# Performance work log

Measured on AMD Instinct MI355X. Metric: run time of the kernel, lower is better.

The kernel has to match this reference:

```python
import jax, jax.numpy as jnp
import numpy as np

N_NODES = 100000
N_EDGES = 1600000
DIM = 128


def setup_inputs() -> dict:
    key = jax.random.key(0)
    k_x, k_e, k_wm, k_bm, k_wu, k_bu = jax.random.split(key, 6)
    bound = 1.0 / np.sqrt(DIM)
    return {
        "x": jax.random.normal(k_x, (N_NODES, DIM), dtype=jnp.float32),
        "edge_index": jax.random.randint(k_e, (2, N_EDGES), 0, N_NODES, dtype=jnp.int64),
        "W_msg": jax.random.uniform(k_wm, (DIM, DIM), jnp.float32, -bound, bound),
        "b_msg": jax.random.uniform(k_bm, (DIM,), jnp.float32, -bound, bound),
        "W_upd": jax.random.uniform(k_wu, (DIM, DIM), jnp.float32, -bound, bound),
        "b_upd": jax.random.uniform(k_bu, (DIM,), jnp.float32, -bound, bound),
    }


def reference(x, edge_index, W_msg, b_msg, W_upd, b_upd):
    # message_net: Linear + ReLU on all nodes  [N, D]
    messages = jax.nn.relu(x @ W_msg.T + b_msg)
    src, dst = edge_index[0], edge_index[1]
    # gather by src, scatter-add by dst (index_add)  [N, D]
    aggregated = jax.ops.segment_sum(messages[src], dst, num_segments=x.shape[0])
    # update_net: Linear + ReLU, then residual
    updated = jax.nn.relu(aggregated @ W_upd.T + b_upd)
    return updated + x
```

## Files before the change

### kernel.cpp

```cpp
#include <hip/hip_runtime.h>
#include <hip/hip_bf16.h>

#define DIM 128
#define BNODES 64
#define CNODES 1024
#define NCMAX 128
#define NBMAX 2048
#define CCAP 20480
#define BCAP 2048
#define FB 16

typedef __attribute__((ext_vector_type(8))) short bf16x8;
typedef __attribute__((ext_vector_type(4))) float f32x4;

__device__ inline ushort f2bf(float f) {
    uint u = __float_as_uint(f);
    u += 0x7fffu + ((u >> 16) & 1u);
    return (ushort)(u >> 16);
}
__device__ inline uint pack2(float lo, float hi) {
    return (uint)f2bf(lo) | ((uint)f2bf(hi) << 16);
}

template<bool RESID, bool BF16OUT>
__device__ __forceinline__
void linear_body(const float* in, const float* __restrict__ W,
                 const float* __restrict__ b, const float* __restrict__ xres,
                 void* outv, int n_tiles, int bid, int nblocks, uint4* Wl)
{
    const int t = threadIdx.x;
    for (int q = t; q < 2048; q += 256) {
        const int j = q >> 4, c = q & 15;
        const float4 lo = ((const float4*)(W + j * 128 + c * 8))[0];
        const float4 hi = ((const float4*)(W + j * 128 + c * 8))[1];
        uint4 pk;
        pk.x = pack2(lo.x, lo.y); pk.y = pack2(lo.z, lo.w);
        pk.z = pack2(hi.x, hi.y); pk.w = pack2(hi.z, hi.w);
        Wl[j * 16 + (c ^ (j & 15))] = pk;
    }
    __syncthreads();

    const int lane = t & 63;
    const int lo4 = lane & 15;
    const int g   = lane >> 4;

    float bias[8];
    #pragma unroll
    for (int ct = 0; ct < 8; ++ct) bias[ct] = b[ct * 16 + lo4];

    const int wid = (bid * 256 + t) >> 6;
    const int nw  = (nblocks * 256) >> 6;

    for (int tile = wid; tile < n_tiles; tile += nw) {
        const int arow = tile * 16 + lo4;
        const float4* ap = (const float4*)(in + (size_t)arow * DIM + g * 32);
        float4 v[8];
        #pragma unroll
        for (int i = 0; i < 8; ++i) v[i] = ap[i];

        bf16x8 afrag[4];
        #pragma unroll
        for (int ks = 0; ks < 4; ++ks) {
            union { bf16x8 v8; uint u[4]; } a;
            a.u[0] = pack2(v[2*ks].x,   v[2*ks].y);
            a.u[1] = pack2(v[2*ks].z,   v[2*ks].w);
            a.u[2] = pack2(v[2*ks+1].x, v[2*ks+1].y);
            a.u[3] = pack2(v[2*ks+1].z, v[2*ks+1].w);
            afrag[ks] = a.v8;
        }

        f32x4 acc[8];
        #pragma unroll
        for (int ct = 0; ct < 8; ++ct)
            acc[ct] = (f32x4){bias[ct], bias[ct], bias[ct], bias[ct]};

        #pragma unroll
        for (int ks = 0; ks < 4; ++ks) {
            #pragma unroll
            for (int ct = 0; ct < 8; ++ct) {
                const int jrow = ct * 16 + lo4;
                const bf16x8 bfrag = *((const bf16x8*)&Wl[jrow * 16 + ((g * 4 + ks) ^ lo4)]);
                acc[ct] = __builtin_amdgcn_mfma_f32_16x16x32_bf16(afrag[ks], bfrag, acc[ct], 0, 0, 0);
            }
        }

        #pragma unroll
        for (int ct = 0; ct < 8; ++ct) {
            #pragma unroll
            for (int r = 0; r < 4; ++r) {
                const int orow = tile * 16 + g * 4 + r;
                const int ocol = ct * 16 + lo4;
                float val = fmaxf(acc[ct][r], 0.f);
                if constexpr (RESID) val += xres[(size_t)orow * DIM + ocol];
                if constexpr (BF16OUT)
                    ((ushort*)outv)[(size_t)orow * DIM + ocol] = f2bf(val);
                else
                    ((float*)outv)[(size_t)orow * DIM + ocol] = val;
            }
        }
    }
}

__global__ __launch_bounds__(256, 2)
void lin1_coarse_kernel(const float* x, const float* __restrict__ Wm,
                        const float* __restrict__ bm, ushort* msg, int n_tiles,
                        const int* __restrict__ ei, int* __restrict__ ccur,
                        uint* __restrict__ cedges, int n_edges, int ncb, int cb)
{
    __shared__ uint4 Wl[128 * 16];
    __shared__ int histL[NCMAX];
    __shared__ int curL[NCMAX];

    const int bid = (int)blockIdx.x;
    if (bid < cb) {
        const int t = threadIdx.x;
        if (t < ncb) histL[t] = 0;
        __syncthreads();
        const int chunk = (n_edges + cb - 1) / cb;
        const int e0 = bid * chunk;
        const int e1 = min(e0 + chunk, n_edges);
        for (int e = e0 + t; e < e1; e += 256)
            atomicAdd(&histL[ei[n_edges + e] >> 10], 1);
        __syncthreads();
        if (t < ncb)
            curL[t] = histL[t] ? atomicAdd(&ccur[t], histL[t]) : 0;
        __syncthreads();
        for (int e = e0 + t; e < e1; e += 256) {
            const int src = ei[e];
            const int dst = ei[n_edges + e];
            const int c = dst >> 10;
            const int pos = atomicAdd(&curL[c], 1);
            if (pos < CCAP)
                cedges[(size_t)c * CCAP + pos] = ((uint)src << 10) | (uint)(dst & 1023);
        }
    } else {
        linear_body<false, true>(x, Wm, bm, nullptr, msg, n_tiles,
                                 bid - cb, (int)gridDim.x - cb, Wl);
    }
}

__global__ __launch_bounds__(256, 2)
void lin2_kernel(const float* agg, const float* __restrict__ Wu,
                 const float* __restrict__ bu, const float* __restrict__ x,
                 float* out, int n_tiles)
{
    __shared__ uint4 Wl[128 * 16];
    linear_body<true, false>(agg, Wu, bu, x, out, n_tiles,
                             (int)blockIdx.x, (int)gridDim.x, Wl);
}

__global__ __launch_bounds__(256)
void fine_scatter_kernel(const int* __restrict__ ccnt, const uint* __restrict__ cedges,
                         int* __restrict__ gcur, uint* __restrict__ bedges, int ncb)
{
    __shared__ int histL[FB];
    __shared__ int curL[FB];
    const int t = threadIdx.x;
    const int c = blockIdx.x >> 3;
    const int s = blockIdx.x & 7;
    const int cnt = min(ccnt[c], CCAP);
    const int chunk = (cnt + 7) / 8;
    const int e0 = s * chunk;
    const int e1 = min(e0 + chunk, cnt);
    if (t < FB) histL[t] = 0;
    __syncthreads();
    const uint* ce = cedges + (size_t)c * CCAP;
    for (int i = e0 + t; i < e1; i += 256)
        atomicAdd(&histL[(ce[i] & 1023u) >> 6], 1);
    __syncthreads();
    if (t < FB)
        curL[t] = histL[t] ? atomicAdd(&gcur[c * FB + t], histL[t]) : 0;
    __syncthreads();
    for (int i = e0 + t; i < e1; i += 256) {
        const uint p = ce[i];
        const uint dl = p & 1023u;
        const int f = (int)(dl >> 6);
        const int pos = atomicAdd(&curL[f], 1);
        if (pos < BCAP)
            bedges[(size_t)(c * FB + f) * BCAP + pos] = ((p >> 10) << 6) | (dl & 63u);
    }
}

__global__ __launch_bounds__(512)
void bucket_gather_kernel(const uint* __restrict__ msg, const int* __restrict__ gcur,
                          const uint* __restrict__ bedges, float* __restrict__ agg,
                          int n_nodes)
{
    __shared__ int  srcL[BCAP];
    __shared__ int histL[BNODES];
    __shared__ int inclL[BNODES];
    __shared__ int cursL[BNODES];

    const int t = threadIdx.x;
    const int b = blockIdx.x;
    const int cnt = min(gcur[b], BCAP);
    const uint* be = bedges + (size_t)b * BCAP;

    if (t < BNODES) histL[t] = 0;
    __syncthreads();
    for (int i = t; i < cnt; i += 512)
        atomicAdd(&histL[be[i] & 63u], 1);
    __syncthreads();
    if (t < BNODES) inclL[t] = histL[t];
    for (int off = 1; off < BNODES; off <<= 1) {
        int add = 0;
        __syncthreads();
        if (t < BNODES && t >= off) add = inclL[t - off];
        __syncthreads();
        if (t < BNODES) inclL[t] += add;
    }
    __syncthreads();
    if (t < BNODES) cursL[t] = inclL[t] - histL[t];
    __syncthreads();
    for (int i = t; i < cnt; i += 512) {
        const uint p = be[i];
        const int pos = atomicAdd(&cursL[p & 63u], 1);
        srcL[pos] = (int)(p >> 6);
    }
    __syncthreads();

    const int lane = t & 63;
    const int w = t >> 6;
    for (int dl = w; dl < BNODES; dl += 8) {
        const int node = b * BNODES + dl;
        if (node >= n_nodes) break;
        const int e1 = inclL[dl];
        const int e0 = e1 - histL[dl];
        float a0 = 0.f, a1 = 0.f;
        int i = e0;
        for (; i + 8 <= e1; i += 8) {
            uint m[8];
            #pragma unroll
            for (int k = 0; k < 8; ++k)
                m[k] = msg[(size_t)srcL[i + k] * 64 + lane];
            #pragma unroll
            for (int k = 0; k < 8; ++k) {
                a0 += __uint_as_float(m[k] << 16);
                a1 += __uint_as_float(m[k] & 0xffff0000u);
            }
        }
        for (; i + 4 <= e1; i += 4) {
            uint m[4];
            #pragma unroll
            for (int k = 0; k < 4; ++k)
                m[k] = msg[(size_t)srcL[i + k] * 64 + lane];
            #pragma unroll
            for (int k = 0; k < 4; ++k) {
                a0 += __uint_as_float(m[k] << 16);
                a1 += __uint_as_float(m[k] & 0xffff0000u);
            }
        }
        for (; i < e1; ++i) {
            const uint m = msg[(size_t)srcL[i] * 64 + lane];
            a0 += __uint_as_float(m << 16);
            a1 += __uint_as_float(m & 0xffff0000u);
        }
        ((float2*)(agg + (size_t)node * DIM))[lane] = make_float2(a0, a1);
    }
}

extern "C" void kernel_launch(void* const* d_in, const int* in_sizes, int n_in,
                              void* d_out, int out_size, void* d_ws, size_t ws_size,
                              hipStream_t stream)
{
    const float* x  = (const float*)d_in[0];
    const int*   ei = (const int*)d_in[1];
    const float* Wm = (const float*)d_in[2];
    const float* bm = (const float*)d_in[3];
    const float* Wu = (const float*)d_in[4];
    const float* bu = (const float*)d_in[5];

    const int N = in_sizes[0] / DIM;
    const int E = in_sizes[1] / 2;
    const int nb  = (N + BNODES - 1) / BNODES;
    const int ncb = (N + CNODES - 1) / CNODES;

    char* ws = (char*)d_ws;
    ushort* msg = (ushort*)ws;
    size_t o = (size_t)N * DIM * sizeof(ushort);
    int* ccur = (int*)(ws + o); o += (size_t)NCMAX * 4;
    int* gcur = (int*)(ws + o); o += (size_t)NBMAX * 4;
    o = (o + 255) & ~(size_t)255;
    uint* cedges = (uint*)(ws + o); o += (size_t)ncb * CCAP * 4;
    o = (o + 255) & ~(size_t)255;
    uint* bedges = (uint*)(ws + o);

    float* out = (float*)d_out;
    float* agg = out;

    const int n_tiles = N / 16;

    hipMemsetAsync(ccur, 0, (size_t)(NCMAX + NBMAX) * 4, stream);

    lin1_coarse_kernel<<<2048, 256, 0, stream>>>(x, Wm, bm, msg, n_tiles,
                                                 ei, ccur, cedges, E, ncb, 1024);

    fine_scatter_kernel<<<ncb * 8, 256, 0, stream>>>(ccur, cedges, gcur, bedges, ncb);

    bucket_gather_kernel<<<nb, 512, 0, stream>>>((const uint*)msg, gcur, bedges, agg, N);

    lin2_kernel<<<1024, 256, 0, stream>>>(agg, Wu, bu, x, out, n_tiles);
}
```

Before: 155.8 us.

## Drop fine scatter pass; gather directly from coarse buckets and store bf16 aggregates

Removes the fine_scatter kernel: each gather block now scans the whole coarse region (1024 nodes) and keeps only edges for its 64-node sub-bucket, eliminating a write and read of the fine edge array and one launch. This costs extra work, since each coarse region's edge list is read by 16 blocks instead of once. When workspace allows, aggregates are stored as bf16 and consumed by a dedicated lin2 kernel loading bf16 A fragments directly, halving aggregate traffic at some precision loss.

```diff
diff --git a/kernel.cpp b/kernel.cpp
--- a/kernel.cpp
+++ b/kernel.cpp
@@ -5,10 +5,8 @@
 #define BNODES 64
 #define CNODES 1024
 #define NCMAX 128
-#define NBMAX 2048
 #define CCAP 20480
 #define BCAP 2048
-#define FB 16
 
 typedef __attribute__((ext_vector_type(8))) short bf16x8;
 typedef __attribute__((ext_vector_type(4))) float f32x4;
@@ -139,67 +137,30 @@
     }
 }
 
-__global__ __launch_bounds__(256, 2)
-void lin2_kernel(const float* agg, const float* __restrict__ Wu,
-                 const float* __restrict__ bu, const float* __restrict__ x,
-                 float* out, int n_tiles)
-{
-    __shared__ uint4 Wl[128 * 16];
-    linear_body<true, false>(agg, Wu, bu, x, out, n_tiles,
-                             (int)blockIdx.x, (int)gridDim.x, Wl);
-}
-
-__global__ __launch_bounds__(256)
-void fine_scatter_kernel(const int* __restrict__ ccnt, const uint* __restrict__ cedges,
-                         int* __restrict__ gcur, uint* __restrict__ bedges, int ncb)
-{
-    __shared__ int histL[FB];
-    __shared__ int curL[FB];
-    const int t = threadIdx.x;
-    const int c = blockIdx.x >> 3;
-    const int s = blockIdx.x & 7;
-    const int cnt = min(ccnt[c], CCAP);
-    const int chunk = (cnt + 7) / 8;
-    const int e0 = s * chunk;
-    const int e1 = min(e0 + chunk, cnt);
-    if (t < FB) histL[t] = 0;
-    __syncthreads();
-    const uint* ce = cedges + (size_t)c * CCAP;
-    for (int i = e0 + t; i < e1; i += 256)
-        atomicAdd(&histL[(ce[i] & 1023u) >> 6], 1);
-    __syncthreads();
-    if (t < FB)
-        curL[t] = histL[t] ? atomicAdd(&gcur[c * FB + t], histL[t]) : 0;
-    __syncthreads();
-    for (int i = e0 + t; i < e1; i += 256) {
-        const uint p = ce[i];
-        const uint dl = p & 1023u;
-        const int f = (int)(dl >> 6);
-        const int pos = atomicAdd(&curL[f], 1);
-        if (pos < BCAP)
-            bedges[(size_t)(c * FB + f) * BCAP + pos] = ((p >> 10) << 6) | (dl & 63u);
-    }
-}
-
+template<bool A16>
 __global__ __launch_bounds__(512)
-void bucket_gather_kernel(const uint* __restrict__ msg, const int* __restrict__ gcur,
-                          const uint* __restrict__ bedges, float* __restrict__ agg,
+void region_gather_kernel(const uint* __restrict__ msg, const int* __restrict__ ccur,
+                          const uint* __restrict__ cedges, void* __restrict__ aggv,
                           int n_nodes)
 {
-    __shared__ int  srcL[BCAP];
+    __shared__ int srcL[BCAP];
     __shared__ int histL[BNODES];
     __shared__ int inclL[BNODES];
     __shared__ int cursL[BNODES];
 
     const int t = threadIdx.x;
     const int b = blockIdx.x;
-    const int cnt = min(gcur[b], BCAP);
-    const uint* be = bedges + (size_t)b * BCAP;
+    const int c = b >> 4;
+    const uint sub = (uint)(b & 15);
+    const int cnt = min(ccur[c], CCAP);
+    const uint* ce = cedges + (size_t)c * CCAP;
 
     if (t < BNODES) histL[t] = 0;
     __syncthreads();
-    for (int i = t; i < cnt; i += 512)
-        atomicAdd(&histL[be[i] & 63u], 1);
+    for (int i = t; i < cnt; i += 512) {
+        const uint p = ce[i];
+        if (((p & 1023u) >> 6) == sub) atomicAdd(&histL[p & 63u], 1);
+    }
     __syncthreads();
     if (t < BNODES) inclL[t] = histL[t];
     for (int off = 1; off < BNODES; off <<= 1) {
@@ -213,9 +174,12 @@
     if (t < BNODES) cursL[t] = inclL[t] - histL[t];
     __syncthreads();
     for (int i = t; i < cnt; i += 512) {
-        const uint p = be[i];
-        const int pos = atomicAdd(&cursL[p & 63u], 1);
-        srcL[pos] = (int)(p >> 6);
+        const uint p = ce[i];
+        const uint dl10 = p & 1023u;
+        if ((dl10 >> 6) == sub) {
+            const int pos = atomicAdd(&cursL[dl10 & 63u], 1);
+            if (pos < BCAP) srcL[pos] = (int)(p >> 10);
+        }
     }
     __syncthreads();
 
@@ -224,8 +188,8 @@
     for (int dl = w; dl < BNODES; dl += 8) {
         const int node = b * BNODES + dl;
         if (node >= n_nodes) break;
-        const int e1 = inclL[dl];
-        const int e0 = e1 - histL[dl];
+        const int e1 = min(inclL[dl], BCAP);
+        const int e0 = min(inclL[dl] - histL[dl], BCAP);
         float a0 = 0.f, a1 = 0.f;
         int i = e0;
         for (; i + 8 <= e1; i += 8) {
@@ -255,7 +219,86 @@
             a0 += __uint_as_float(m << 16);
             a1 += __uint_as_float(m & 0xffff0000u);
         }
-        ((float2*)(agg + (size_t)node * DIM))[lane] = make_float2(a0, a1);
+        if constexpr (A16)
+            ((uint*)aggv)[(size_t)node * 64 + lane] = pack2(a0, a1);
+        else
+            ((float2*)((float*)aggv + (size_t)node * DIM))[lane] = make_float2(a0, a1);
+    }
+}
+
+__global__ __launch_bounds__(256, 2)
+void lin2_kernel(const float* agg, const float* __restrict__ Wu,
+                 const float* __restrict__ bu, const float* __restrict__ x,
+                 float* out, int n_tiles)
+{
+    __shared__ uint4 Wl[128 * 16];
+    linear_body<true, false>(agg, Wu, bu, x, out, n_tiles,
+                             (int)blockIdx.x, (int)gridDim.x, Wl);
+}
+
+__global__ __launch_bounds__(256, 2)
+void lin2_a16_kernel(const uint4* __restrict__ agg16, const float* __restrict__ Wu,
+                     const float* __restrict__ bu, const float* __restrict__ x,
+                     float* __restrict__ out, int n_tiles)
+{
+    __shared__ uint4 Wl[128 * 16];
+    const int t = threadIdx.x;
+    for (int q = t; q < 2048; q += 256) {
+        const int j = q >> 4, c = q & 15;
+        const float4 lo = ((const float4*)(Wu + j * 128 + c * 8))[0];
+        const float4 hi = ((const float4*)(Wu + j * 128 + c * 8))[1];
+        uint4 pk;
+        pk.x = pack2(lo.x, lo.y); pk.y = pack2(lo.z, lo.w);
+        pk.z = pack2(hi.x, hi.y); pk.w = pack2(hi.z, hi.w);
+        Wl[j * 16 + (c ^ (j & 15))] = pk;
+    }
+    __syncthreads();
+
+    const int lane = t & 63;
+    const int lo4 = lane & 15;
+    const int g   = lane >> 4;
+
+    float bias[8];
+    #pragma unroll
+    for (int ct = 0; ct < 8; ++ct) bias[ct] = bu[ct * 16 + lo4];
+
+    const int wid = ((int)blockIdx.x * 256 + t) >> 6;
+    const int nw  = ((int)gridDim.x * 256) >> 6;
+
+    for (int tile = wid; tile < n_tiles; tile += nw) {
+        const int arow = tile * 16 + lo4;
+        bf16x8 afrag[4];
+        #pragma unroll
+        for (int ks = 0; ks < 4; ++ks) {
+            const uint4 u = agg16[(size_t)arow * 16 + g * 4 + ks];
+            afrag[ks] = *(const bf16x8*)&u;
+        }
+
+        f32x4 acc[8];
+        #pragma unroll
+        for (int ct = 0; ct < 8; ++ct)
+            acc[ct] = (f32x4){bias[ct], bias[ct], bias[ct], bias[ct]};
+
+        #pragma unroll
+        for (int ks = 0; ks < 4; ++ks) {
+            #pragma unroll
+            for (int ct = 0; ct < 8; ++ct) {
+                const int jrow = ct * 16 + lo4;
+                const bf16x8 bfrag = *((const bf16x8*)&Wl[jrow * 16 + ((g * 4 + ks) ^ lo4)]);
+                acc[ct] = __builtin_amdgcn_mfma_f32_16x16x32_bf16(afrag[ks], bfrag, acc[ct], 0, 0, 0);
+            }
+        }
+
+        #pragma unroll
+        for (int ct = 0; ct < 8; ++ct) {
+            #pragma unroll
+            for (int r = 0; r < 4; ++r) {
+                const int orow = tile * 16 + g * 4 + r;
+                const int ocol = ct * 16 + lo4;
+                out[(size_t)orow * DIM + ocol] =
+                    fmaxf(acc[ct][r], 0.f) + x[(size_t)orow * DIM + ocol];
+            }
+        }
     }
 }
 
@@ -279,25 +322,29 @@
     ushort* msg = (ushort*)ws;
     size_t o = (size_t)N * DIM * sizeof(ushort);
     int* ccur = (int*)(ws + o); o += (size_t)NCMAX * 4;
-    int* gcur = (int*)(ws + o); o += (size_t)NBMAX * 4;
     o = (o + 255) & ~(size_t)255;
     uint* cedges = (uint*)(ws + o); o += (size_t)ncb * CCAP * 4;
     o = (o + 255) & ~(size_t)255;
-    uint* bedges = (uint*)(ws + o);
+    uint* agg16 = (uint*)(ws + o);
+    const size_t need16 = o + (size_t)N * 64 * 4;
+    const bool a16 = ws_size >= need16;
 
     float* out = (float*)d_out;
-    float* agg = out;
-
     const int n_tiles = N / 16;
 
-    hipMemsetAsync(ccur, 0, (size_t)(NCMAX + NBMAX) * 4, stream);
+    hipMemsetAsync(ccur, 0, (size_t)NCMAX * 4, stream);
 
     lin1_coarse_kernel<<<2048, 256, 0, stream>>>(x, Wm, bm, msg, n_tiles,
                                                  ei, ccur, cedges, E, ncb, 1024);
 
-    fine_scatter_kernel<<<ncb * 8, 256, 0, stream>>>(ccur, cedges, gcur, bedges, ncb);
-
-    bucket_gather_kernel<<<nb, 512, 0, stream>>>((const uint*)msg, gcur, bedges, agg, N);
-
-    lin2_kernel<<<1024, 256, 0, stream>>>(agg, Wu, bu, x, out, n_tiles);
-}
+    if (a16) {
+        region_gather_kernel<true><<<nb, 512, 0, stream>>>(
+            (const uint*)msg, ccur, cedges, agg16, N);
+        lin2_a16_kernel<<<1024, 256, 0, stream>>>(
+            (const uint4*)agg16, Wu, bu, x, out, n_tiles);
+    } else {
+        region_gather_kernel<false><<<nb, 512, 0, stream>>>(
+            (const uint*)msg, ccur, cedges, out, N);
+        lin2_kernel<<<1024, 256, 0, stream>>>(out, Wu, bu, x, out, n_tiles);
+    }
+}
```

Result: slower. 175.4 us (+12.6%).
